# Optimization experiments

Hardware: AMD Instinct MI355X
Metric: run time of the kernel (lower is better)

Reference implementation:

```python
import jax, jax.numpy as jnp
import numpy as np

N_NODES = 50000
N_EDGES = 800000
IN_DIM = 256
HID = 64
HEADS = [4, 4, 1]
N_CLASSES = 16
SLOPE = 0.2


def mish(x):
    return x * jnp.tanh(jax.nn.softplus(x))


def gat_conv(x, src, dst, W, attn_l, attn_r, bias, res_W, n_heads, d_out, act):
    """DGL GATConv (feat_drop=attn_drop=0, residual=True, bias=True).
    x: (N, F_in); src/dst: (E,) edge endpoints; message flows src -> dst.
    """
    N = x.shape[0]
    feat = (x @ W).reshape(N, n_heads, d_out)            # (N, H, D)
    el = jnp.sum(feat * attn_l, axis=-1)                 # (N, H)
    er = jnp.sum(feat * attn_r, axis=-1)                 # (N, H)
    e = jax.nn.leaky_relu(el[src] + er[dst], SLOPE)      # (E, H)
    # segment softmax over incoming edges of each dst node
    emax = jax.ops.segment_max(e, dst, num_segments=N)   # (N, H)
    ee = jnp.exp(e - emax[dst])                          # (E, H)
    denom = jax.ops.segment_sum(ee, dst, num_segments=N) # (N, H)
    a = ee / denom[dst]                                  # (E, H)
    # weighted scatter-aggregate of source features
    rst = jax.ops.segment_sum(feat[src] * a[:, :, None], dst, num_segments=N)  # (N, H, D)
    # residual: identity if F_in == H*D else linear projection (DGL semantics)
    if res_W is None:
        res = x.reshape(N, n_heads, d_out)
    else:
        res = (x @ res_W).reshape(N, n_heads, d_out)
    rst = rst + res + bias.reshape(1, n_heads, d_out)
    if act:
        rst = mish(rst)
    return rst


def setup_inputs() -> dict:
    key = jax.random.key(0)
    ks = jax.random.split(key, 16)
    x = jax.random.normal(ks[0], (N_NODES, IN_DIM), dtype=jnp.float32)
    src = jax.random.randint(ks[1], (N_EDGES,), 0, N_NODES, dtype=jnp.int32)
    dst = jax.random.randint(ks[2], (N_EDGES,), 0, N_NODES, dtype=jnp.int32)
    s = 0.1
    # layer 0: 256 -> 4 heads x 64
    W0 = jax.random.normal(ks[3], (IN_DIM, HEADS[0] * HID), jnp.float32) * s
    al0 = jax.random.normal(ks[4], (HEADS[0], HID), jnp.float32) * s
    ar0 = jax.random.normal(ks[5], (HEADS[0], HID), jnp.float32) * s
    b0 = jnp.zeros((HEADS[0] * HID,), jnp.float32)
    # layer 1: 256 -> 4 heads x 64
    W1 = jax.random.normal(ks[6], (HEADS[0] * HID, HEADS[1] * HID), jnp.float32) * s
    al1 = jax.random.normal(ks[7], (HEADS[1], HID), jnp.float32) * s
    ar1 = jax.random.normal(ks[8], (HEADS[1], HID), jnp.float32) * s
    b1 = jnp.zeros((HEADS[1] * HID,), jnp.float32)
    # output layer: 256 -> 1 head x 16 (residual needs a linear projection)
    W2 = jax.random.normal(ks[9], (HEADS[1] * HID, HEADS[2] * N_CLASSES), jnp.float32) * s
    al2 = jax.random.normal(ks[10], (HEADS[2], N_CLASSES), jnp.float32) * s
    ar2 = jax.random.normal(ks[11], (HEADS[2], N_CLASSES), jnp.float32) * s
    b2 = jnp.zeros((HEADS[2] * N_CLASSES,), jnp.float32)
    resW2 = jax.random.normal(ks[12], (HEADS[1] * HID, HEADS[2] * N_CLASSES), jnp.float32) * s
    return {"x": x, "src": src, "dst": dst,
            "W0": W0, "al0": al0, "ar0": ar0, "b0": b0,
            "W1": W1, "al1": al1, "ar1": ar1, "b1": b1,
            "W2": W2, "al2": al2, "ar2": ar2, "b2": b2, "resW2": resW2}


def reference(x, src, dst, W0, al0, ar0, b0, W1, al1, ar1, b1, W2, al2, ar2, b2, resW2):
    N = x.shape[0]
    h = gat_conv(x, src, dst, W0, al0, ar0, b0, None, HEADS[0], HID, True).reshape(N, -1)
    h = gat_conv(h, src, dst, W1, al1, ar1, b1, None, HEADS[1], HID, True).reshape(N, -1)
    logits = gat_conv(h, src, dst, W2, al2, ar2, b2, resW2, HEADS[2], N_CLASSES, False).mean(axis=1)
    return logits
```

## Files before the change

kernel.cpp:

```cpp
#include <hip/hip_runtime.h>
#include <cmath>
#include <type_traits>

typedef __bf16 bf16;
typedef __attribute__((ext_vector_type(8))) __bf16 bf16x8;
typedef __attribute__((ext_vector_type(4))) __bf16 bf16x4;
typedef __attribute__((ext_vector_type(4))) float f32x4;

__device__ __forceinline__ unsigned f2s(float x) {
    unsigned u = __float_as_uint(x);
    return (u & 0x80000000u) ? ~u : (u | 0x80000000u);
}
__device__ __forceinline__ float s2f(unsigned s) {
    return (s & 0x80000000u) ? __uint_as_float(s & 0x7FFFFFFFu)
                             : __uint_as_float(~s);
}

__global__ void prep_weights_kernel(const float* __restrict__ W0, const float* __restrict__ W1,
                                    const float* __restrict__ W2, const float* __restrict__ rW2,
                                    bf16* __restrict__ Wt0, bf16* __restrict__ Wt1,
                                    bf16* __restrict__ Bct) {
    const int idx = blockIdx.x * blockDim.x + threadIdx.x;
    if (idx < 65536) {
        const int k = idx >> 8, m = idx & 255;
        Wt0[m * 256 + k] = (bf16)W0[idx];
        Wt1[m * 256 + k] = (bf16)W1[idx];
    }
    if (idx < 8192) {
        const int m = idx >> 8, k = idx & 255;
        const float v = (m < 16) ? W2[k * 16 + m] : rW2[k * 16 + (m - 16)];
        Bct[idx] = (bf16)v;
    }
}

template <typename AT>
__global__ __launch_bounds__(256) void gemm_mfma_bf16(const AT* __restrict__ A,
                                                      const bf16* __restrict__ Bt,
                                                      bf16* __restrict__ Fb, int N) {
    constexpr int K = 256, BM = 128, BK = 32;
    constexpr int LDA = BK + 8;
    __shared__ bf16 As[BM * LDA];
    __shared__ bf16 Bs[BM * LDA];

    const int tid = threadIdx.x;
    const int wave = tid >> 6, lane = tid & 63;
    const int quad = lane >> 4, l16 = lane & 15;
    const int rowBase = blockIdx.y * BM;
    const int colBase = blockIdx.x * BM;
    const int m_base = (wave >> 1) * 64, n_base = (wave & 1) * 64;

    f32x4 acc[4][4] = {};

    const int sr = tid >> 1;
    const int seg = (tid & 1) << 4;

    for (int k0 = 0; k0 < K; k0 += BK) {
        {
            const int gr = rowBase + sr;
            if constexpr (std::is_same<AT, float>::value) {
                float4 f0 = {0,0,0,0}, f1 = {0,0,0,0}, f2 = {0,0,0,0}, f3 = {0,0,0,0};
                if (gr < N) {
                    const float4* Ag = (const float4*)(A + (long)gr * K + k0 + seg);
                    f0 = Ag[0]; f1 = Ag[1]; f2 = Ag[2]; f3 = Ag[3];
                }
                bf16x8 p0, p1;
                p0[0] = (bf16)f0.x; p0[1] = (bf16)f0.y; p0[2] = (bf16)f0.z; p0[3] = (bf16)f0.w;
                p0[4] = (bf16)f1.x; p0[5] = (bf16)f1.y; p0[6] = (bf16)f1.z; p0[7] = (bf16)f1.w;
                p1[0] = (bf16)f2.x; p1[1] = (bf16)f2.y; p1[2] = (bf16)f2.z; p1[3] = (bf16)f2.w;
                p1[4] = (bf16)f3.x; p1[5] = (bf16)f3.y; p1[6] = (bf16)f3.z; p1[7] = (bf16)f3.w;
                *(bf16x8*)&As[sr * LDA + seg] = p0;
                *(bf16x8*)&As[sr * LDA + seg + 8] = p1;
            } else {
                bf16x8 p0 = {}, p1 = {};
                if (gr < N) {
                    const bf16x8* Ag = (const bf16x8*)(A + (long)gr * K + k0 + seg);
                    p0 = Ag[0]; p1 = Ag[1];
                }
                *(bf16x8*)&As[sr * LDA + seg] = p0;
                *(bf16x8*)&As[sr * LDA + seg + 8] = p1;
            }
        }
        {
            const bf16x8* Bg = (const bf16x8*)(Bt + (long)(colBase + sr) * K + k0 + seg);
            *(bf16x8*)&Bs[sr * LDA + seg] = Bg[0];
            *(bf16x8*)&Bs[sr * LDA + seg + 8] = Bg[1];
        }
        __syncthreads();

        bf16x8 af[4], bfr[4];
#pragma unroll
        for (int mi = 0; mi < 4; mi++)
            af[mi] = *(const bf16x8*)&As[(m_base + mi * 16 + l16) * LDA + quad * 8];
#pragma unroll
        for (int ni = 0; ni < 4; ni++)
            bfr[ni] = *(const bf16x8*)&Bs[(n_base + ni * 16 + l16) * LDA + quad * 8];
#pragma unroll
        for (int mi = 0; mi < 4; mi++)
#pragma unroll
            for (int ni = 0; ni < 4; ni++)
                acc[mi][ni] = __builtin_amdgcn_mfma_f32_16x16x32_bf16(af[mi], bfr[ni], acc[mi][ni], 0, 0, 0);
        __syncthreads();
    }

#pragma unroll
    for (int mi = 0; mi < 4; mi++) {
#pragma unroll
        for (int r = 0; r < 4; r++) {
            const int grow = rowBase + m_base + mi * 16 + quad * 4 + r;
            if (grow < N) {
#pragma unroll
                for (int ni = 0; ni < 4; ni++) {
                    Fb[(long)grow * 256 + colBase + n_base + ni * 16 + l16] = (bf16)acc[mi][ni][r];
                }
            }
        }
    }
}

__global__ __launch_bounds__(256) void gemm_mfma_n32(const bf16* __restrict__ A,
                                                     const bf16* __restrict__ Bt,
                                                     float* __restrict__ C, int N) {
    constexpr int K = 256, BM = 128, BK = 32;
    constexpr int LDA = BK + 8;
    __shared__ bf16 As[BM * LDA];
    __shared__ bf16 Bs[32 * LDA];

    const int tid = threadIdx.x;
    const int wave = tid >> 6, lane = tid & 63;
    const int quad = lane >> 4, l16 = lane & 15;
    const int rowBase = blockIdx.x * BM;
    const int m_base = (wave >> 1) * 64, n_base = (wave & 1) * 16;

    f32x4 acc[4] = {};

    const int sr = tid >> 1;
    const int seg = (tid & 1) << 4;

    for (int k0 = 0; k0 < K; k0 += BK) {
        {
            const int gr = rowBase + sr;
            bf16x8 p0 = {}, p1 = {};
            if (gr < N) {
                const bf16x8* Ag = (const bf16x8*)(A + (long)gr * K + k0 + seg);
                p0 = Ag[0]; p1 = Ag[1];
            }
            *(bf16x8*)&As[sr * LDA + seg] = p0;
            *(bf16x8*)&As[sr * LDA + seg + 8] = p1;
        }
        if (tid < 64) {
            const int br = tid >> 1;
            const bf16x8* Bg = (const bf16x8*)(Bt + br * K + k0 + seg);
            *(bf16x8*)&Bs[br * LDA + seg] = Bg[0];
            *(bf16x8*)&Bs[br * LDA + seg + 8] = Bg[1];
        }
        __syncthreads();

        const bf16x8 bfr = *(const bf16x8*)&Bs[(n_base + l16) * LDA + quad * 8];
#pragma unroll
        for (int mi = 0; mi < 4; mi++) {
            const bf16x8 af = *(const bf16x8*)&As[(m_base + mi * 16 + l16) * LDA + quad * 8];
            acc[mi] = __builtin_amdgcn_mfma_f32_16x16x32_bf16(af, bfr, acc[mi], 0, 0, 0);
        }
        __syncthreads();
    }

#pragma unroll
    for (int mi = 0; mi < 4; mi++) {
#pragma unroll
        for (int r = 0; r < 4; r++) {
            const int grow = rowBase + m_base + mi * 16 + quad * 4 + r;
            if (grow < N) C[(long)grow * 32 + n_base + l16] = acc[mi][r];
        }
    }
}

__global__ void el_er_node_kernel(const bf16* __restrict__ feat,
                                  const float* __restrict__ al, const float* __restrict__ ar,
                                  float* __restrict__ el, float* __restrict__ er, int N) {
    const int wid = (blockIdx.x * blockDim.x + threadIdx.x) >> 6;
    const int lane = threadIdx.x & 63;
    if (wid >= N) return;
    const bf16x4 f = ((const bf16x4*)feat)[(long)wid * 64 + lane];
    const float4 a = ((const float4*)al)[lane];
    const float4 b = ((const float4*)ar)[lane];
    const float f0 = (float)f[0], f1 = (float)f[1], f2 = (float)f[2], f3 = (float)f[3];
    float vl = f0 * a.x + f1 * a.y + f2 * a.z + f3 * a.w;
    float vr = f0 * b.x + f1 * b.y + f2 * b.z + f3 * b.w;
#pragma unroll
    for (int off = 1; off < 16; off <<= 1) {
        vl += __shfl_xor(vl, off);
        vr += __shfl_xor(vr, off);
    }
    if ((lane & 15) == 0) {
        const int h = lane >> 4;
        el[wid * 4 + h] = vl;
        er[wid * 4 + h] = vr;
    }
}

__global__ void el_er_strided16(const float* __restrict__ feat, int stride,
                                const float* __restrict__ al, const float* __restrict__ ar,
                                float* __restrict__ el, float* __restrict__ er, int N) {
    const int wid = (blockIdx.x * blockDim.x + threadIdx.x) >> 6;
    const int lane = threadIdx.x & 63;
    if (wid >= N) return;
    float vl = 0.f, vr = 0.f;
    if (lane < 16) {
        float f = feat[(long)wid * stride + lane];
        vl = f * al[lane];
        vr = f * ar[lane];
    }
#pragma unroll
    for (int off = 1; off < 16; off <<= 1) {
        vl += __shfl_xor(vl, off);
        vr += __shfl_xor(vr, off);
    }
    if (lane == 0) { el[wid] = vl; er[wid] = vr; }
}

__global__ void elmax4_kernel(const float4* __restrict__ el4, unsigned* __restrict__ elmax_u, int n4) {
    __shared__ float4 sm[256];
    float4 m = {-INFINITY, -INFINITY, -INFINITY, -INFINITY};
    for (int i = blockIdx.x * blockDim.x + threadIdx.x; i < n4; i += gridDim.x * blockDim.x) {
        const float4 v = el4[i];
        m.x = fmaxf(m.x, v.x); m.y = fmaxf(m.y, v.y);
        m.z = fmaxf(m.z, v.z); m.w = fmaxf(m.w, v.w);
    }
    sm[threadIdx.x] = m;
    __syncthreads();
    for (int off = 128; off > 0; off >>= 1) {
        if (threadIdx.x < off) {
            float4 o = sm[threadIdx.x + off];
            float4 c = sm[threadIdx.x];
            c.x = fmaxf(c.x, o.x); c.y = fmaxf(c.y, o.y);
            c.z = fmaxf(c.z, o.z); c.w = fmaxf(c.w, o.w);
            sm[threadIdx.x] = c;
        }
        __syncthreads();
    }
    if (threadIdx.x == 0) {
        const float4 r = sm[0];
        atomicMax(&elmax_u[0], f2s(r.x));
        atomicMax(&elmax_u[1], f2s(r.y));
        atomicMax(&elmax_u[2], f2s(r.z));
        atomicMax(&elmax_u[3], f2s(r.w));
    }
}


__global__ void count_deg_kernel(const int* __restrict__ dst, int* __restrict__ deg, int E) {
    const int e = blockIdx.x * blockDim.x + threadIdx.x;
    if (e >= E) return;
    atomicAdd(&deg[dst[e]], 1);
}

__global__ void scan_block_kernel(const int* __restrict__ deg, int* __restrict__ scanned,
                                  int* __restrict__ block_sums, int N) {
    __shared__ int smem[256];
    const int tid = threadIdx.x;
    const int base = blockIdx.x * 1024 + tid * 4;
    int v[4];
#pragma unroll
    for (int i = 0; i < 4; i++) v[i] = (base + i < N) ? deg[base + i] : 0;
    const int tsum = v[0] + v[1] + v[2] + v[3];
    smem[tid] = tsum;
    __syncthreads();
    int acc = tsum;
    for (int off = 1; off < 256; off <<= 1) {
        const int t = (tid >= off) ? smem[tid - off] : 0;
        __syncthreads();
        acc += t;
        smem[tid] = acc;
        __syncthreads();
    }
    if (tid == 255) block_sums[blockIdx.x] = acc;
    int run = acc - tsum;
#pragma unroll
    for (int i = 0; i < 4; i++) {
        if (base + i < N) scanned[base + i] = run;
        run += v[i];
    }
}

__global__ void scan_sums_kernel(int* __restrict__ block_sums, unsigned* __restrict__ elmax_u, int nb) {
    const int tid = threadIdx.x;
    if (tid < 12) elmax_u[tid] = f2s(-INFINITY);
    const int orig = (tid < nb) ? block_sums[tid] : 0;
    int v = orig;
#pragma unroll
    for (int off = 1; off < 64; off <<= 1) {
        const int t = __shfl_up(v, off);
        if (tid >= off) v += t;
    }
    if (tid < nb) block_sums[tid] = v - orig;
}

__global__ void apply_offsets_kernel(const int* __restrict__ scanned, const int* __restrict__ block_sums,
                                     int* __restrict__ row_ptr, int* __restrict__ cursor, int N, int E) {
    const int i = blockIdx.x * blockDim.x + threadIdx.x;
    if (i < N) {
        const int v = scanned[i] + block_sums[i >> 10];
        row_ptr[i] = v;
        cursor[i] = v;
    }
    if (i == 0) row_ptr[N] = E;
}

__global__ void scatter_kernel(const int* __restrict__ src, const int* __restrict__ dst,
                               int* __restrict__ cursor, int* __restrict__ csr_src, int E) {
    const int e = blockIdx.x * blockDim.x + threadIdx.x;
    if (e >= E) return;
    const int pos = atomicAdd(&cursor[dst[e]], 1);
    csr_src[pos] = src[e];
}

template <int H, int D, bool ACT, typename RT, typename OT>
__global__ void gat_aggregate_wave(const int* __restrict__ row_ptr, const int* __restrict__ csr_src,
                                   const float* __restrict__ el, const float* __restrict__ er,
                                   const unsigned* __restrict__ elmax_u,
                                   const bf16* __restrict__ feat,
                                   const RT* __restrict__ res, const float* __restrict__ bias,
                                   OT* __restrict__ out, int N) {
    constexpr int C = H * D;
    constexpr int V = C / 4;
    const int wave = threadIdx.x >> 6;
    const int lane = threadIdx.x & 63;
    int n = blockIdx.x * (blockDim.x >> 6) + wave;
    if (n >= N) return;
    n = __builtin_amdgcn_readfirstlane(n);
    const int h = lane >> 4;
    const bf16x4* feat4 = (const bf16x4*)feat;

    const float erd = er[n * H + h];
    float sh = s2f(elmax_u[h]) + erd;
    sh = (sh >= 0.f) ? sh : 0.2f * sh;

    float4 acc = {0.f, 0.f, 0.f, 0.f};
    float l = 0.f;
    int p = row_ptr[n];
    const int pend = row_ptr[n + 1];
    for (; p + 4 <= pend; p += 4) {
        const int s0 = csr_src[p + 0];
        const int s1 = csr_src[p + 1];
        const int s2 = csr_src[p + 2];
        const int s3 = csr_src[p + 3];
        float e0 = el[s0 * H + h] + erd;
        float e1 = el[s1 * H + h] + erd;
        float e2 = el[s2 * H + h] + erd;
        float e3 = el[s3 * H + h] + erd;
        e0 = (e0 >= 0.f) ? e0 : 0.2f * e0;
        e1 = (e1 >= 0.f) ? e1 : 0.2f * e1;
        e2 = (e2 >= 0.f) ? e2 : 0.2f * e2;
        e3 = (e3 >= 0.f) ? e3 : 0.2f * e3;
        const float w0 = __expf(e0 - sh);
        const float w1 = __expf(e1 - sh);
        const float w2 = __expf(e2 - sh);
        const float w3 = __expf(e3 - sh);
        const bf16x4 f0 = feat4[(long)s0 * V + lane];
        const bf16x4 f1 = feat4[(long)s1 * V + lane];
        const bf16x4 f2 = feat4[(long)s2 * V + lane];
        const bf16x4 f3 = feat4[(long)s3 * V + lane];
        l += w0 + w1 + w2 + w3;
        acc.x += w0 * (float)f0[0] + w1 * (float)f1[0] + w2 * (float)f2[0] + w3 * (float)f3[0];
        acc.y += w0 * (float)f0[1] + w1 * (float)f1[1] + w2 * (float)f2[1] + w3 * (float)f3[1];
        acc.z += w0 * (float)f0[2] + w1 * (float)f1[2] + w2 * (float)f2[2] + w3 * (float)f3[2];
        acc.w += w0 * (float)f0[3] + w1 * (float)f1[3] + w2 * (float)f2[3] + w3 * (float)f3[3];
    }
    for (; p < pend; ++p) {
        const int s = csr_src[p];
        float e = el[s * H + h] + erd;
        e = (e >= 0.f) ? e : 0.2f * e;
        const float w = __expf(e - sh);
        const bf16x4 f = feat4[(long)s * V + lane];
        l += w;
        acc.x += w * (float)f[0];
        acc.y += w * (float)f[1];
        acc.z += w * (float)f[2];
        acc.w += w * (float)f[3];
    }
    const float inv = (l > 0.f) ? 1.f / l : 0.f;
    acc.x *= inv; acc.y *= inv; acc.z *= inv; acc.w *= inv;

    float4 r;
    if constexpr (std::is_same<RT, float>::value) {
        r = ((const float4*)res)[(long)n * V + lane];
    } else {
        const bf16x4 rb = ((const bf16x4*)res)[(long)n * V + lane];
        r = make_float4((float)rb[0], (float)rb[1], (float)rb[2], (float)rb[3]);
    }
    const float4 bb = ((const float4*)bias)[lane];
    float v[4] = {acc.x + r.x + bb.x, acc.y + r.y + bb.y,
                  acc.z + r.z + bb.z, acc.w + r.w + bb.w};
    if (ACT) {
#pragma unroll
        for (int i = 0; i < 4; i++) {
            const float sp = (v[i] > 20.f) ? v[i] : log1pf(expf(v[i]));
            v[i] = v[i] * tanhf(sp);
        }
    }
    if constexpr (std::is_same<OT, float>::value) {
        float4 o = {v[0], v[1], v[2], v[3]};
        ((float4*)out)[(long)n * V + lane] = o;
    } else {
        bf16x4 o;
        o[0] = (bf16)v[0]; o[1] = (bf16)v[1]; o[2] = (bf16)v[2]; o[3] = (bf16)v[3];
        ((bf16x4*)out)[(long)n * V + lane] = o;
    }
}

template <bool ACT, int NPB>
__global__ void gat_aggregate_small(const int* __restrict__ row_ptr, const int* __restrict__ csr_src,
                                    const float* __restrict__ el, const float* __restrict__ er,
                                    const unsigned* __restrict__ elmax_u,
                                    const float* __restrict__ feat, int fstride,
                                    const float* __restrict__ res, int rstride,
                                    const float* __restrict__ bias, float* __restrict__ out, int N) {
    constexpr int C = 16;
    const int local = threadIdx.x % C;
    const int n = blockIdx.x * NPB + threadIdx.x / C;
    if (n >= N) return;
    const float mx = fmaxf(fmaxf(s2f(elmax_u[8]), s2f(elmax_u[9])),
                           fmaxf(s2f(elmax_u[10]), s2f(elmax_u[11])));
    const float erd = er[n];
    float sh = mx + erd;
    sh = (sh >= 0.f) ? sh : 0.2f * sh;

    float acc = 0.f, l = 0.f;
    int p = row_ptr[n];
    const int pend = row_ptr[n + 1];
    for (; p + 4 <= pend; p += 4) {
        const int s0 = csr_src[p + 0];
        const int s1 = csr_src[p + 1];
        const int s2 = csr_src[p + 2];
        const int s3 = csr_src[p + 3];
        float e0 = el[s0] + erd, e1 = el[s1] + erd, e2 = el[s2] + erd, e3 = el[s3] + erd;
        e0 = (e0 >= 0.f) ? e0 : 0.2f * e0;
        e1 = (e1 >= 0.f) ? e1 : 0.2f * e1;
        e2 = (e2 >= 0.f) ? e2 : 0.2f * e2;
        e3 = (e3 >= 0.f) ? e3 : 0.2f * e3;
        const float w0 = __expf(e0 - sh);
        const float w1 = __expf(e1 - sh);
        const float w2 = __expf(e2 - sh);
        const float w3 = __expf(e3 - sh);
        l += w0 + w1 + w2 + w3;
        acc += w0 * feat[(long)s0 * fstride + local] + w1 * feat[(long)s1 * fstride + local]
             + w2 * feat[(long)s2 * fstride + local] + w3 * feat[(long)s3 * fstride + local];
    }
    for (; p < pend; ++p) {
        const int s = csr_src[p];
        float e = el[s] + erd;
        e = (e >= 0.f) ? e : 0.2f * e;
        const float w = __expf(e - sh);
        l += w;
        acc += w * feat[(long)s * fstride + local];
    }
    const float inv = (l > 0.f) ? 1.f / l : 0.f;
    float v = acc * inv + res[(long)n * rstride + local] + bias[local];
    if (ACT) {
        const float sp = (v > 20.f) ? v : log1pf(expf(v));
        v = v * tanhf(sp);
    }
    out[(long)n * C + local] = v;
}


static inline int cdiv(long a, long b) { return (int)((a + b - 1) / b); }

extern "C" void kernel_launch(void* const* d_in, const int* in_sizes, int n_in,
                              void* d_out, int out_size, void* d_ws, size_t ws_size,
                              hipStream_t stream) {
    const float* x   = (const float*)d_in[0];
    const int*   src = (const int*)d_in[1];
    const int*   dst = (const int*)d_in[2];
    const float* W0  = (const float*)d_in[3];
    const float* al0 = (const float*)d_in[4];
    const float* ar0 = (const float*)d_in[5];
    const float* b0  = (const float*)d_in[6];
    const float* W1  = (const float*)d_in[7];
    const float* al1 = (const float*)d_in[8];
    const float* ar1 = (const float*)d_in[9];
    const float* b1  = (const float*)d_in[10];
    const float* W2  = (const float*)d_in[11];
    const float* al2 = (const float*)d_in[12];
    const float* ar2 = (const float*)d_in[13];
    const float* b2  = (const float*)d_in[14];
    const float* rW2 = (const float*)d_in[15];
    float* out = (float*)d_out;

    const int N = in_sizes[0] / 256;
    const int E = in_sizes[1];

    bf16* Wt0    = (bf16*)d_ws;
    bf16* Wt1    = Wt0 + 65536;
    bf16* Bct    = Wt1 + 65536;
    bf16* Fb     = Bct + 8192;
    bf16* Hb     = Fb + (long)N * 256;
    float* F2    = (float*)(Hb + (long)N * 256);
    float* el    = F2 + (long)N * 32;
    float* er    = el + (long)N * 4;
    unsigned* elmax_u = (unsigned*)(er + (long)N * 4);
    int* deg     = (int*)(elmax_u + 12);
    int* scanned = deg + N;
    int* bsums   = scanned + N;
    int* row_ptr = bsums + 64;
    int* cursor  = row_ptr + N + 1;
    int* csr_src = cursor + N;

    const int THREADS = 256;
    const int NB = cdiv(N, 1024);
    dim3 mfma_grid(2, cdiv(N, 128));

    prep_weights_kernel<<<cdiv(65536, THREADS), THREADS, 0, stream>>>(W0, W1, W2, rW2, Wt0, Wt1, Bct);
    hipMemsetAsync(deg, 0, (size_t)N * 4, stream);
    count_deg_kernel<<<cdiv(E, THREADS), THREADS, 0, stream>>>(dst, deg, E);
    scan_block_kernel<<<NB, 256, 0, stream>>>(deg, scanned, bsums, N);
    scan_sums_kernel<<<1, 64, 0, stream>>>(bsums, elmax_u, NB);
    apply_offsets_kernel<<<cdiv(N, THREADS), THREADS, 0, stream>>>(scanned, bsums, row_ptr, cursor, N, E);
    scatter_kernel<<<cdiv(E, THREADS), THREADS, 0, stream>>>(src, dst, cursor, csr_src, E);

    gemm_mfma_bf16<float><<<mfma_grid, 256, 0, stream>>>(x, Wt0, Fb, N);
    el_er_node_kernel<<<cdiv(N, 4), 256, 0, stream>>>(Fb, al0, ar0, el, er, N);
    elmax4_kernel<<<64, 256, 0, stream>>>((const float4*)el, elmax_u, N);
    gat_aggregate_wave<4, 64, true, float, bf16><<<cdiv(N, 4), 256, 0, stream>>>(
        row_ptr, csr_src, el, er, elmax_u, Fb, x, b0, Hb, N);

    gemm_mfma_bf16<bf16><<<mfma_grid, 256, 0, stream>>>(Hb, Wt1, Fb, N);
    el_er_node_kernel<<<cdiv(N, 4), 256, 0, stream>>>(Fb, al1, ar1, el, er, N);
    elmax4_kernel<<<64, 256, 0, stream>>>((const float4*)el, elmax_u + 4, N);
    gat_aggregate_wave<4, 64, true, bf16, bf16><<<cdiv(N, 4), 256, 0, stream>>>(
        row_ptr, csr_src, el, er, elmax_u + 4, Fb, Hb, b1, Hb, N);

    gemm_mfma_n32<<<cdiv(N, 128), 256, 0, stream>>>(Hb, Bct, F2, N);
    el_er_strided16<<<cdiv(N, 4), 256, 0, stream>>>(F2, 32, al2, ar2, el, er, N);
    elmax4_kernel<<<64, 256, 0, stream>>>((const float4*)el, elmax_u + 8, N / 4);
    gat_aggregate_small<false, 16><<<cdiv(N, 16), 256, 0, stream>>>(row_ptr, csr_src, el, er, elmax_u,
                                                                    F2, 32, F2 + 16, 32, b2, out, N);
}
```

Measured before the change: 477.6 us.

## Fuse el/er with max reduction, pack two nodes per wave, use exp2

Several changes land together. Attention logits are computed and max-reduced in one grid-stride kernel, which removes the separate elmax kernels. LOG2E is folded into the attention weights so the softmax can use exp2f. x is cast to bf16 once up front, and the deg memset is folded into the weight-prep kernel. The aggregation kernel now handles two destination nodes per wave with 8-wide bf16 loads, which cuts launches, global traffic and per-node wave underuse. The risks are lane divergence when the paired nodes have unequal degree, and an extra kernel plus buffer for the x cast.

```diff
diff --git a/kernel.cpp b/kernel.cpp
--- a/kernel.cpp
+++ b/kernel.cpp
@@ -7,6 +7,8 @@
 typedef __attribute__((ext_vector_type(4))) __bf16 bf16x4;
 typedef __attribute__((ext_vector_type(4))) float f32x4;
 
+#define LOG2E 1.4426950408889634f
+
 __device__ __forceinline__ unsigned f2s(float x) {
     unsigned u = __float_as_uint(x);
     return (u & 0x80000000u) ? ~u : (u | 0x80000000u);
@@ -19,7 +21,7 @@
 __global__ void prep_weights_kernel(const float* __restrict__ W0, const float* __restrict__ W1,
                                     const float* __restrict__ W2, const float* __restrict__ rW2,
                                     bf16* __restrict__ Wt0, bf16* __restrict__ Wt1,
-                                    bf16* __restrict__ Bct) {
+                                    bf16* __restrict__ Bct, int* __restrict__ deg, int N) {
     const int idx = blockIdx.x * blockDim.x + threadIdx.x;
     if (idx < 65536) {
         const int k = idx >> 8, m = idx & 255;
@@ -31,10 +33,21 @@
         const float v = (m < 16) ? W2[k * 16 + m] : rW2[k * 16 + (m - 16)];
         Bct[idx] = (bf16)v;
     }
-}
-
-template <typename AT>
-__global__ __launch_bounds__(256) void gemm_mfma_bf16(const AT* __restrict__ A,
+    if (idx < N) deg[idx] = 0;
+}
+
+__global__ void cast_x_kernel(const float* __restrict__ x, bf16* __restrict__ xb, long total8) {
+    const long t = (long)blockIdx.x * blockDim.x + threadIdx.x;
+    if (t >= total8) return;
+    const float4* xp = (const float4*)x + t * 2;
+    const float4 f0 = xp[0], f1 = xp[1];
+    bf16x8 o;
+    o[0] = (bf16)f0.x; o[1] = (bf16)f0.y; o[2] = (bf16)f0.z; o[3] = (bf16)f0.w;
+    o[4] = (bf16)f1.x; o[5] = (bf16)f1.y; o[6] = (bf16)f1.z; o[7] = (bf16)f1.w;
+    ((bf16x8*)xb)[t] = o;
+}
+
+__global__ __launch_bounds__(256) void gemm_mfma_bf16(const bf16* __restrict__ A,
                                                       const bf16* __restrict__ Bt,
                                                       bf16* __restrict__ Fb, int N) {
     constexpr int K = 256, BM = 128, BK = 32;
@@ -50,88 +63,6 @@
     const int m_base = (wave >> 1) * 64, n_base = (wave & 1) * 64;
 
     f32x4 acc[4][4] = {};
-
-    const int sr = tid >> 1;
-    const int seg = (tid & 1) << 4;
-
-    for (int k0 = 0; k0 < K; k0 += BK) {
-        {
-            const int gr = rowBase + sr;
-            if constexpr (std::is_same<AT, float>::value) {
-                float4 f0 = {0,0,0,0}, f1 = {0,0,0,0}, f2 = {0,0,0,0}, f3 = {0,0,0,0};
-                if (gr < N) {
-                    const float4* Ag = (const float4*)(A + (long)gr * K + k0 + seg);
-                    f0 = Ag[0]; f1 = Ag[1]; f2 = Ag[2]; f3 = Ag[3];
-                }
-                bf16x8 p0, p1;
-                p0[0] = (bf16)f0.x; p0[1] = (bf16)f0.y; p0[2] = (bf16)f0.z; p0[3] = (bf16)f0.w;
-                p0[4] = (bf16)f1.x; p0[5] = (bf16)f1.y; p0[6] = (bf16)f1.z; p0[7] = (bf16)f1.w;
-                p1[0] = (bf16)f2.x; p1[1] = (bf16)f2.y; p1[2] = (bf16)f2.z; p1[3] = (bf16)f2.w;
-                p1[4] = (bf16)f3.x; p1[5] = (bf16)f3.y; p1[6] = (bf16)f3.z; p1[7] = (bf16)f3.w;
-                *(bf16x8*)&As[sr * LDA + seg] = p0;
-                *(bf16x8*)&As[sr * LDA + seg + 8] = p1;
-            } else {
-                bf16x8 p0 = {}, p1 = {};
-                if (gr < N) {
-                    const bf16x8* Ag = (const bf16x8*)(A + (long)gr * K + k0 + seg);
-                    p0 = Ag[0]; p1 = Ag[1];
-                }
-                *(bf16x8*)&As[sr * LDA + seg] = p0;
-                *(bf16x8*)&As[sr * LDA + seg + 8] = p1;
-            }
-        }
-        {
-            const bf16x8* Bg = (const bf16x8*)(Bt + (long)(colBase + sr) * K + k0 + seg);
-            *(bf16x8*)&Bs[sr * LDA + seg] = Bg[0];
-            *(bf16x8*)&Bs[sr * LDA + seg + 8] = Bg[1];
-        }
-        __syncthreads();
-
-        bf16x8 af[4], bfr[4];
-#pragma unroll
-        for (int mi = 0; mi < 4; mi++)
-            af[mi] = *(const bf16x8*)&As[(m_base + mi * 16 + l16) * LDA + quad * 8];
-#pragma unroll
-        for (int ni = 0; ni < 4; ni++)
-            bfr[ni] = *(const bf16x8*)&Bs[(n_base + ni * 16 + l16) * LDA + quad * 8];
-#pragma unroll
-        for (int mi = 0; mi < 4; mi++)
-#pragma unroll
-            for (int ni = 0; ni < 4; ni++)
-                acc[mi][ni] = __builtin_amdgcn_mfma_f32_16x16x32_bf16(af[mi], bfr[ni], acc[mi][ni], 0, 0, 0);
-        __syncthreads();
-    }
-
-#pragma unroll
-    for (int mi = 0; mi < 4; mi++) {
-#pragma unroll
-        for (int r = 0; r < 4; r++) {
-            const int grow = rowBase + m_base + mi * 16 + quad * 4 + r;
-            if (grow < N) {
-#pragma unroll
-                for (int ni = 0; ni < 4; ni++) {
-                    Fb[(long)grow * 256 + colBase + n_base + ni * 16 + l16] = (bf16)acc[mi][ni][r];
-                }
-            }
-        }
-    }
-}
-
-__global__ __launch_bounds__(256) void gemm_mfma_n32(const bf16* __restrict__ A,
-                                                     const bf16* __restrict__ Bt,
-                                                     float* __restrict__ C, int N) {
-    constexpr int K = 256, BM = 128, BK = 32;
-    constexpr int LDA = BK + 8;
-    __shared__ bf16 As[BM * LDA];
-    __shared__ bf16 Bs[32 * LDA];
-
-    const int tid = threadIdx.x;
-    const int wave = tid >> 6, lane = tid & 63;
-    const int quad = lane >> 4, l16 = lane & 15;
-    const int rowBase = blockIdx.x * BM;
-    const int m_base = (wave >> 1) * 64, n_base = (wave & 1) * 16;
-
-    f32x4 acc[4] = {};
 
     const int sr = tid >> 1;
     const int seg = (tid & 1) << 4;
@@ -147,6 +78,73 @@
             *(bf16x8*)&As[sr * LDA + seg] = p0;
             *(bf16x8*)&As[sr * LDA + seg + 8] = p1;
         }
+        {
+            const bf16x8* Bg = (const bf16x8*)(Bt + (long)(colBase + sr) * K + k0 + seg);
+            *(bf16x8*)&Bs[sr * LDA + seg] = Bg[0];
+            *(bf16x8*)&Bs[sr * LDA + seg + 8] = Bg[1];
+        }
+        __syncthreads();
+
+        bf16x8 af[4], bfr[4];
+#pragma unroll
+        for (int mi = 0; mi < 4; mi++)
+            af[mi] = *(const bf16x8*)&As[(m_base + mi * 16 + l16) * LDA + quad * 8];
+#pragma unroll
+        for (int ni = 0; ni < 4; ni++)
+            bfr[ni] = *(const bf16x8*)&Bs[(n_base + ni * 16 + l16) * LDA + quad * 8];
+#pragma unroll
+        for (int mi = 0; mi < 4; mi++)
+#pragma unroll
+            for (int ni = 0; ni < 4; ni++)
+                acc[mi][ni] = __builtin_amdgcn_mfma_f32_16x16x32_bf16(af[mi], bfr[ni], acc[mi][ni], 0, 0, 0);
+        __syncthreads();
+    }
+
+#pragma unroll
+    for (int mi = 0; mi < 4; mi++) {
+#pragma unroll
+        for (int r = 0; r < 4; r++) {
+            const int grow = rowBase + m_base + mi * 16 + quad * 4 + r;
+            if (grow < N) {
+#pragma unroll
+                for (int ni = 0; ni < 4; ni++) {
+                    Fb[(long)grow * 256 + colBase + n_base + ni * 16 + l16] = (bf16)acc[mi][ni][r];
+                }
+            }
+        }
+    }
+}
+
+__global__ __launch_bounds__(256) void gemm_mfma_n32(const bf16* __restrict__ A,
+                                                     const bf16* __restrict__ Bt,
+                                                     float* __restrict__ C, int N) {
+    constexpr int K = 256, BM = 128, BK = 32;
+    constexpr int LDA = BK + 8;
+    __shared__ bf16 As[BM * LDA];
+    __shared__ bf16 Bs[32 * LDA];
+
+    const int tid = threadIdx.x;
+    const int wave = tid >> 6, lane = tid & 63;
+    const int quad = lane >> 4, l16 = lane & 15;
+    const int rowBase = blockIdx.x * BM;
+    const int m_base = (wave >> 1) * 64, n_base = (wave & 1) * 16;
+
+    f32x4 acc[4] = {};
+
+    const int sr = tid >> 1;
+    const int seg = (tid & 1) << 4;
+
+    for (int k0 = 0; k0 < K; k0 += BK) {
+        {
+            const int gr = rowBase + sr;
+            bf16x8 p0 = {}, p1 = {};
+            if (gr < N) {
+                const bf16x8* Ag = (const bf16x8*)(A + (long)gr * K + k0 + seg);
+                p0 = Ag[0]; p1 = Ag[1];
+            }
+            *(bf16x8*)&As[sr * LDA + seg] = p0;
+            *(bf16x8*)&As[sr * LDA + seg + 8] = p1;
+        }
         if (tid < 64) {
             const int br = tid >> 1;
             const bf16x8* Bg = (const bf16x8*)(Bt + br * K + k0 + seg);
@@ -174,76 +172,82 @@
     }
 }
 
-__global__ void el_er_node_kernel(const bf16* __restrict__ feat,
-                                  const float* __restrict__ al, const float* __restrict__ ar,
-                                  float* __restrict__ el, float* __restrict__ er, int N) {
-    const int wid = (blockIdx.x * blockDim.x + threadIdx.x) >> 6;
+__global__ void el_er_fused(const bf16* __restrict__ feat,
+                            const float* __restrict__ al, const float* __restrict__ ar,
+                            float* __restrict__ el, float* __restrict__ er,
+                            unsigned* __restrict__ elmax_u, int N) {
+    __shared__ float smax[16];
+    const int wave = threadIdx.x >> 6;
     const int lane = threadIdx.x & 63;
-    if (wid >= N) return;
-    const bf16x4 f = ((const bf16x4*)feat)[(long)wid * 64 + lane];
-    const float4 a = ((const float4*)al)[lane];
-    const float4 b = ((const float4*)ar)[lane];
-    const float f0 = (float)f[0], f1 = (float)f[1], f2 = (float)f[2], f3 = (float)f[3];
-    float vl = f0 * a.x + f1 * a.y + f2 * a.z + f3 * a.w;
-    float vr = f0 * b.x + f1 * b.y + f2 * b.z + f3 * b.w;
-#pragma unroll
-    for (int off = 1; off < 16; off <<= 1) {
-        vl += __shfl_xor(vl, off);
-        vr += __shfl_xor(vr, off);
-    }
-    if ((lane & 15) == 0) {
-        const int h = lane >> 4;
-        el[wid * 4 + h] = vl;
-        er[wid * 4 + h] = vr;
-    }
-}
-
-__global__ void el_er_strided16(const float* __restrict__ feat, int stride,
-                                const float* __restrict__ al, const float* __restrict__ ar,
-                                float* __restrict__ el, float* __restrict__ er, int N) {
-    const int wid = (blockIdx.x * blockDim.x + threadIdx.x) >> 6;
+    const int h = lane >> 4;
+    float4 a = ((const float4*)al)[lane];
+    float4 b = ((const float4*)ar)[lane];
+    a.x *= LOG2E; a.y *= LOG2E; a.z *= LOG2E; a.w *= LOG2E;
+    b.x *= LOG2E; b.y *= LOG2E; b.z *= LOG2E; b.w *= LOG2E;
+    const int nwaves = (gridDim.x * blockDim.x) >> 6;
+    float mloc = -INFINITY;
+    for (int wid = (blockIdx.x * blockDim.x + threadIdx.x) >> 6; wid < N; wid += nwaves) {
+        const bf16x4 f = ((const bf16x4*)feat)[(long)wid * 64 + lane];
+        const float f0 = (float)f[0], f1 = (float)f[1], f2 = (float)f[2], f3 = (float)f[3];
+        float vl = f0 * a.x + f1 * a.y + f2 * a.z + f3 * a.w;
+        float vr = f0 * b.x + f1 * b.y + f2 * b.z + f3 * b.w;
+#pragma unroll
+        for (int off = 1; off < 16; off <<= 1) {
+            vl += __shfl_xor(vl, off);
+            vr += __shfl_xor(vr, off);
+        }
+        if ((lane & 15) == 0) {
+            el[wid * 4 + h] = vl;
+            er[wid * 4 + h] = vr;
+            mloc = fmaxf(mloc, vl);
+        }
+    }
+    if ((lane & 15) == 0) smax[wave * 4 + h] = mloc;
+    __syncthreads();
+    if (threadIdx.x < 4) {
+        const float m = fmaxf(fmaxf(smax[threadIdx.x], smax[4 + threadIdx.x]),
+                              fmaxf(smax[8 + threadIdx.x], smax[12 + threadIdx.x]));
+        atomicMax(&elmax_u[threadIdx.x], f2s(m));
+    }
+}
+
+__global__ void el_er2_fused(const float* __restrict__ F2,
+                             const float* __restrict__ al2, const float* __restrict__ ar2,
+                             float* __restrict__ el, float* __restrict__ er,
+                             unsigned* __restrict__ elmax_u, int N) {
+    __shared__ float smax[4];
+    const int wave = threadIdx.x >> 6;
     const int lane = threadIdx.x & 63;
-    if (wid >= N) return;
-    float vl = 0.f, vr = 0.f;
-    if (lane < 16) {
-        float f = feat[(long)wid * stride + lane];
-        vl = f * al[lane];
-        vr = f * ar[lane];
-    }
-#pragma unroll
-    for (int off = 1; off < 16; off <<= 1) {
-        vl += __shfl_xor(vl, off);
-        vr += __shfl_xor(vr, off);
-    }
-    if (lane == 0) { el[wid] = vl; er[wid] = vr; }
-}
-
-__global__ void elmax4_kernel(const float4* __restrict__ el4, unsigned* __restrict__ elmax_u, int n4) {
-    __shared__ float4 sm[256];
-    float4 m = {-INFINITY, -INFINITY, -INFINITY, -INFINITY};
-    for (int i = blockIdx.x * blockDim.x + threadIdx.x; i < n4; i += gridDim.x * blockDim.x) {
-        const float4 v = el4[i];
-        m.x = fmaxf(m.x, v.x); m.y = fmaxf(m.y, v.y);
-        m.z = fmaxf(m.z, v.z); m.w = fmaxf(m.w, v.w);
-    }
-    sm[threadIdx.x] = m;
+    const int sub = lane >> 4;
+    const int c = lane & 15;
+    const float a = al2[c] * LOG2E;
+    const float b = ar2[c] * LOG2E;
+    const int nwaves = (gridDim.x * blockDim.x) >> 6;
+    float mloc = -INFINITY;
+    for (int q = (blockIdx.x * blockDim.x + threadIdx.x) >> 6; q * 4 < N; q += nwaves) {
+        const int n = q * 4 + sub;
+        float vl = 0.f, vr = 0.f;
+        if (n < N) {
+            const float f = F2[(long)n * 32 + c];
+            vl = f * a; vr = f * b;
+        }
+#pragma unroll
+        for (int off = 1; off < 16; off <<= 1) {
+            vl += __shfl_xor(vl, off);
+            vr += __shfl_xor(vr, off);
+        }
+        if (c == 0 && n < N) {
+            el[n] = vl; er[n] = vr;
+            mloc = fmaxf(mloc, vl);
+        }
+    }
+    mloc = fmaxf(mloc, __shfl_xor(mloc, 16));
+    mloc = fmaxf(mloc, __shfl_xor(mloc, 32));
+    if (lane == 0) smax[wave] = mloc;
     __syncthreads();
-    for (int off = 128; off > 0; off >>= 1) {
-        if (threadIdx.x < off) {
-            float4 o = sm[threadIdx.x + off];
-            float4 c = sm[threadIdx.x];
-            c.x = fmaxf(c.x, o.x); c.y = fmaxf(c.y, o.y);
-            c.z = fmaxf(c.z, o.z); c.w = fmaxf(c.w, o.w);
-            sm[threadIdx.x] = c;
-        }
-        __syncthreads();
-    }
     if (threadIdx.x == 0) {
-        const float4 r = sm[0];
-        atomicMax(&elmax_u[0], f2s(r.x));
-        atomicMax(&elmax_u[1], f2s(r.y));
-        atomicMax(&elmax_u[2], f2s(r.z));
-        atomicMax(&elmax_u[3], f2s(r.w));
+        const float m = fmaxf(fmaxf(smax[0], smax[1]), fmaxf(smax[2], smax[3]));
+        atomicMax(&elmax_u[8], f2s(m));
     }
 }
 
@@ -314,97 +318,105 @@
     csr_src[pos] = src[e];
 }
 
-template <int H, int D, bool ACT, typename RT, typename OT>
-__global__ void gat_aggregate_wave(const int* __restrict__ row_ptr, const int* __restrict__ csr_src,
-                                   const float* __restrict__ el, const float* __restrict__ er,
-                                   const unsigned* __restrict__ elmax_u,
-                                   const bf16* __restrict__ feat,
-                                   const RT* __restrict__ res, const float* __restrict__ bias,
-                                   OT* __restrict__ out, int N) {
-    constexpr int C = H * D;
-    constexpr int V = C / 4;
+template <bool ACT>
+__global__ void gat_aggregate_wave2(const int* __restrict__ row_ptr, const int* __restrict__ csr_src,
+                                    const float* __restrict__ el, const float* __restrict__ er,
+                                    const unsigned* __restrict__ elmax_u,
+                                    const bf16* __restrict__ feat,
+                                    const bf16* __restrict__ res, const float* __restrict__ bias,
+                                    bf16* __restrict__ out, int N, int E) {
     const int wave = threadIdx.x >> 6;
     const int lane = threadIdx.x & 63;
-    int n = blockIdx.x * (blockDim.x >> 6) + wave;
-    if (n >= N) return;
-    n = __builtin_amdgcn_readfirstlane(n);
-    const int h = lane >> 4;
-    const bf16x4* feat4 = (const bf16x4*)feat;
-
-    const float erd = er[n * H + h];
+    const int half = lane >> 5;
+    const int li   = lane & 31;
+    const int h    = li >> 3;
+    int nA = (blockIdx.x * (blockDim.x >> 6) + wave) * 2;
+    if (nA >= N) return;
+    nA = __builtin_amdgcn_readfirstlane(nA);
+    const int nB = nA + 1;
+    const bool haveB = (nB < N);
+    const int n = half ? (haveB ? nB : nA) : nA;
+
+    const float erd = er[n * 4 + h];
     float sh = s2f(elmax_u[h]) + erd;
-    sh = (sh >= 0.f) ? sh : 0.2f * sh;
-
-    float4 acc = {0.f, 0.f, 0.f, 0.f};
+    sh = fmaxf(sh, 0.2f * sh);
+
+    const int pA0 = row_ptr[nA];
+    const int pA1 = row_ptr[nA + 1];
+    const int pB0 = haveB ? row_ptr[nB] : 0;
+    const int pB1 = haveB ? row_ptr[nB + 1] : 0;
+    const int degA = pA1 - pA0, degB = pB1 - pB0;
+    const int steps = (degA > degB) ? degA : degB;
+    const int deg = half ? degB : degA;
+
+    const bf16x8* feat8 = (const bf16x8*)feat;
+    float acc[8] = {};
     float l = 0.f;
-    int p = row_ptr[n];
-    const int pend = row_ptr[n + 1];
-    for (; p + 4 <= pend; p += 4) {
-        const int s0 = csr_src[p + 0];
-        const int s1 = csr_src[p + 1];
-        const int s2 = csr_src[p + 2];
-        const int s3 = csr_src[p + 3];
-        float e0 = el[s0 * H + h] + erd;
-        float e1 = el[s1 * H + h] + erd;
-        float e2 = el[s2 * H + h] + erd;
-        float e3 = el[s3 * H + h] + erd;
-        e0 = (e0 >= 0.f) ? e0 : 0.2f * e0;
-        e1 = (e1 >= 0.f) ? e1 : 0.2f * e1;
-        e2 = (e2 >= 0.f) ? e2 : 0.2f * e2;
-        e3 = (e3 >= 0.f) ? e3 : 0.2f * e3;
-        const float w0 = __expf(e0 - sh);
-        const float w1 = __expf(e1 - sh);
-        const float w2 = __expf(e2 - sh);
-        const float w3 = __expf(e3 - sh);
-        const bf16x4 f0 = feat4[(long)s0 * V + lane];
-        const bf16x4 f1 = feat4[(long)s1 * V + lane];
-        const bf16x4 f2 = feat4[(long)s2 * V + lane];
-        const bf16x4 f3 = feat4[(long)s3 * V + lane];
-        l += w0 + w1 + w2 + w3;
-        acc.x += w0 * (float)f0[0] + w1 * (float)f1[0] + w2 * (float)f2[0] + w3 * (float)f3[0];
-        acc.y += w0 * (float)f0[1] + w1 * (float)f1[1] + w2 * (float)f2[1] + w3 * (float)f3[1];
-        acc.z += w0 * (float)f0[2] + w1 * (float)f1[2] + w2 * (float)f2[2] + w3 * (float)f3[2];
-        acc.w += w0 * (float)f0[3] + w1 * (float)f1[3] + w2 * (float)f2[3] + w3 * (float)f3[3];
-    }
-    for (; p < pend; ++p) {
-        const int s = csr_src[p];
-        float e = el[s * H + h] + erd;
-        e = (e >= 0.f) ? e : 0.2f * e;
-        const float w = __expf(e - sh);
-        const bf16x4 f = feat4[(long)s * V + lane];
+
+    int i = 0;
+    for (; i + 2 <= steps; i += 2) {
+        const int iA0 = min(pA0 + i, E - 1);
+        const int iB0 = min(pB0 + i, E - 1);
+        const int iA1 = min(pA0 + i + 1, E - 1);
+        const int iB1 = min(pB0 + i + 1, E - 1);
+        const int sA0 = csr_src[iA0], sB0 = csr_src[iB0];
+        const int sA1 = csr_src[iA1], sB1 = csr_src[iB1];
+        const int s0 = half ? sB0 : sA0;
+        const int s1 = half ? sB1 : sA1;
+        float e0 = el[s0 * 4 + h] + erd;
+        float e1 = el[s1 * 4 + h] + erd;
+        e0 = fmaxf(e0, 0.2f * e0);
+        e1 = fmaxf(e1, 0.2f * e1);
+        float w0 = exp2f(e0 - sh);
+        float w1 = exp2f(e1 - sh);
+        w0 = (i < deg) ? w0 : 0.f;
+        w1 = (i + 1 < deg) ? w1 : 0.f;
+        const bf16x8 f0 = feat8[(long)s0 * 32 + li];
+        const bf16x8 f1 = feat8[(long)s1 * 32 + li];
+        l += w0 + w1;
+#pragma unroll
+        for (int j = 0; j < 8; j++) acc[j] += w0 * (float)f0[j] + w1 * (float)f1[j];
+    }
+    for (; i < steps; ++i) {
+        const int iA = min(pA0 + i, E - 1);
+        const int iB = min(pB0 + i, E - 1);
+        const int sA = csr_src[iA], sB = csr_src[iB];
+        const int s = half ? sB : sA;
+        float e = el[s * 4 + h] + erd;
+        e = fmaxf(e, 0.2f * e);
+        float w = exp2f(e - sh);
+        w = (i < deg) ? w : 0.f;
+        const bf16x8 f = feat8[(long)s * 32 + li];
         l += w;
-        acc.x += w * (float)f[0];
-        acc.y += w * (float)f[1];
-        acc.z += w * (float)f[2];
-        acc.w += w * (float)f[3];
+#pragma unroll
+        for (int j = 0; j < 8; j++) acc[j] += w * (float)f[j];
     }
     const float inv = (l > 0.f) ? 1.f / l : 0.f;
-    acc.x *= inv; acc.y *= inv; acc.z *= inv; acc.w *= inv;
-
-    float4 r;
-    if constexpr (std::is_same<RT, float>::value) {
-        r = ((const float4*)res)[(long)n * V + lane];
-    } else {
-        const bf16x4 rb = ((const bf16x4*)res)[(long)n * V + lane];
-        r = make_float4((float)rb[0], (float)rb[1], (float)rb[2], (float)rb[3]);
-    }
-    const float4 bb = ((const float4*)bias)[lane];
-    float v[4] = {acc.x + r.x + bb.x, acc.y + r.y + bb.y,
-                  acc.z + r.z + bb.z, acc.w + r.w + bb.w};
+
+    const bf16x8 rb = ((const bf16x8*)res)[(long)n * 32 + li];
+    const float4 bb0 = ((const float4*)bias)[li * 2];
+    const float4 bb1 = ((const float4*)bias)[li * 2 + 1];
+    float v[8];
+    v[0] = acc[0] * inv + (float)rb[0] + bb0.x;
+    v[1] = acc[1] * inv + (float)rb[1] + bb0.y;
+    v[2] = acc[2] * inv + (float)rb[2] + bb0.z;
+    v[3] = acc[3] * inv + (float)rb[3] + bb0.w;
+    v[4] = acc[4] * inv + (float)rb[4] + bb1.x;
+    v[5] = acc[5] * inv + (float)rb[5] + bb1.y;
+    v[6] = acc[6] * inv + (float)rb[6] + bb1.z;
+    v[7] = acc[7] * inv + (float)rb[7] + bb1.w;
     if (ACT) {
 #pragma unroll
-        for (int i = 0; i < 4; i++) {
-            const float sp = (v[i] > 20.f) ? v[i] : log1pf(expf(v[i]));
-            v[i] = v[i] * tanhf(sp);
-        }
-    }
-    if constexpr (std::is_same<OT, float>::value) {
-        float4 o = {v[0], v[1], v[2], v[3]};
-        ((float4*)out)[(long)n * V + lane] = o;
-    } else {
-        bf16x4 o;
-        o[0] = (bf16)v[0]; o[1] = (bf16)v[1]; o[2] = (bf16)v[2]; o[3] = (bf16)v[3];
-        ((bf16x4*)out)[(long)n * V + lane] = o;
+        for (int j = 0; j < 8; j++) {
+            const float sp = (v[j] > 20.f) ? v[j] : log1pf(expf(v[j]));
+            v[j] = v[j] * tanhf(sp);
+        }
+    }
+    if (half == 0 || haveB) {
+        bf16x8 o;
+#pragma unroll
+        for (int j = 0; j < 8; j++) o[j] = (bf16)v[j];
+        ((bf16x8*)out)[(long)n * 32 + li] = o;
     }
 }
 
@@ -419,11 +431,10 @@
     const int local = threadIdx.x % C;
     const int n = blockIdx.x * NPB + threadIdx.x / C;
     if (n >= N) return;
-    const float mx = fmaxf(fmaxf(s2f(elmax_u[8]), s2f(elmax_u[9])),
-                           fmaxf(s2f(elmax_u[10]), s2f(elmax_u[11])));
+    const float mx = s2f(elmax_u[8]);
     const float erd = er[n];
     float sh = mx + erd;
-    sh = (sh >= 0.f) ? sh : 0.2f * sh;
+    sh = fmaxf(sh, 0.2f * sh);
 
     float acc = 0.f, l = 0.f;
     int p = row_ptr[n];
@@ -434,14 +445,14 @@
         const int s2 = csr_src[p + 2];
         const int s3 = csr_src[p + 3];
         float e0 = el[s0] + erd, e1 = el[s1] + erd, e2 = el[s2] + erd, e3 = el[s3] + erd;
-        e0 = (e0 >= 0.f) ? e0 : 0.2f * e0;
-        e1 = (e1 >= 0.f) ? e1 : 0.2f * e1;
-        e2 = (e2 >= 0.f) ? e2 : 0.2f * e2;
-        e3 = (e3 >= 0.f) ? e3 : 0.2f * e3;
-        const float w0 = __expf(e0 - sh);
-        const float w1 = __expf(e1 - sh);
-        const float w2 = __expf(e2 - sh);
-        const float w3 = __expf(e3 - sh);
+        e0 = fmaxf(e0, 0.2f * e0);
+        e1 = fmaxf(e1, 0.2f * e1);
+        e2 = fmaxf(e2, 0.2f * e2);
+        e3 = fmaxf(e3, 0.2f * e3);
+        const float w0 = exp2f(e0 - sh);
+        const float w1 = exp2f(e1 - sh);
+        const float w2 = exp2f(e2 - sh);
+        const float w3 = exp2f(e3 - sh);
         l += w0 + w1 + w2 + w3;
         acc += w0 * feat[(long)s0 * fstride + local] + w1 * feat[(long)s1 * fstride + local]
              + w2 * feat[(long)s2 * fstride + local] + w3 * feat[(long)s3 * fstride + local];
@@ -449,8 +460,8 @@
     for (; p < pend; ++p) {
         const int s = csr_src[p];
         float e = el[s] + erd;
-        e = (e >= 0.f) ? e : 0.2f * e;
-        const float w = __expf(e - sh);
+        e = fmaxf(e, 0.2f * e);
+        const float w = exp2f(e - sh);
         l += w;
         acc += w * feat[(long)s * fstride + local];
     }
@@ -493,7 +504,8 @@
     bf16* Wt0    = (bf16*)d_ws;
     bf16* Wt1    = Wt0 + 65536;
     bf16* Bct    = Wt1 + 65536;
-    bf16* Fb     = Bct + 8192;
+    bf16* xb     = Bct + 8192;
+    bf16* Fb     = xb + (long)N * 256;
     bf16* Hb     = Fb + (long)N * 256;
     float* F2    = (float*)(Hb + (long)N * 256);
     float* el    = F2 + (long)N * 32;
@@ -510,29 +522,26 @@
     const int NB = cdiv(N, 1024);
     dim3 mfma_grid(2, cdiv(N, 128));
 
-    prep_weights_kernel<<<cdiv(65536, THREADS), THREADS, 0, stream>>>(W0, W1, W2, rW2, Wt0, Wt1, Bct);
-    hipMemsetAsync(deg, 0, (size_t)N * 4, stream);
+    prep_weights_kernel<<<cdiv(65536, THREADS), THREADS, 0, stream>>>(W0, W1, W2, rW2, Wt0, Wt1, Bct, deg, N);
+    cast_x_kernel<<<cdiv((long)N * 32, THREADS), THREADS, 0, stream>>>(x, xb, (long)N * 32);
     count_deg_kernel<<<cdiv(E, THREADS), THREADS, 0, stream>>>(dst, deg, E);
     scan_block_kernel<<<NB, 256, 0, stream>>>(deg, scanned, bsums, N);
     scan_sums_kernel<<<1, 64, 0, stream>>>(bsums, elmax_u, NB);
     apply_offsets_kernel<<<cdiv(N, THREADS), THREADS, 0, stream>>>(scanned, bsums, row_ptr, cursor, N, E);
     scatter_kernel<<<cdiv(E, THREADS), THREADS, 0, stream>>>(src, dst, cursor, csr_src, E);
 
-    gemm_mfma_bf16<float><<<mfma_grid, 256, 0, stream>>>(x, Wt0, Fb, N);
-    el_er_node_kernel<<<cdiv(N, 4), 256, 0, stream>>>(Fb, al0, ar0, el, er, N);
-    elmax4_kernel<<<64, 256, 0, stream>>>((const float4*)el, elmax_u, N);
-    gat_aggregate_wave<4, 64, true, float, bf16><<<cdiv(N, 4), 256, 0, stream>>>(
-        row_ptr, csr_src, el, er, elmax_u, Fb, x, b0, Hb, N);
-
-    gemm_mfma_bf16<bf16><<<mfma_grid, 256, 0, stream>>>(Hb, Wt1, Fb, N);
-    el_er_node_kernel<<<cdiv(N, 4), 256, 0, stream>>>(Fb, al1, ar1, el, er, N);
-    elmax4_kernel<<<64, 256, 0, stream>>>((const float4*)el, elmax_u + 4, N);
-    gat_aggregate_wave<4, 64, true, bf16, bf16><<<cdiv(N, 4), 256, 0, stream>>>(
-        row_ptr, csr_src, el, er, elmax_u + 4, Fb, Hb, b1, Hb, N);
+    gemm_mfma_bf16<<<mfma_grid, 256, 0, stream>>>(xb, Wt0, Fb, N);
+    el_er_fused<<<256, 256, 0, stream>>>(Fb, al0, ar0, el, er, elmax_u, N);
+    gat_aggregate_wave2<true><<<cdiv(N, 8), 256, 0, stream>>>(
+        row_ptr, csr_src, el, er, elmax_u, Fb, xb, b0, Hb, N, E);
+
+    gemm_mfma_bf16<<<mfma_grid, 256, 0, stream>>>(Hb, Wt1, Fb, N);
+    el_er_fused<<<256, 256, 0, stream>>>(Fb, al1, ar1, el, er, elmax_u + 4, N);
+    gat_aggregate_wave2<true><<<cdiv(N, 8), 256, 0, stream>>>(
+        row_ptr, csr_src, el, er, elmax_u + 4, Fb, Hb, b1, Hb, N, E);
 
     gemm_mfma_n32<<<cdiv(N, 128), 256, 0, stream>>>(Hb, Bct, F2, N);
-    el_er_strided16<<<cdiv(N, 4), 256, 0, stream>>>(F2, 32, al2, ar2, el, er, N);
-    elmax4_kernel<<<64, 256, 0, stream>>>((const float4*)el, elmax_u + 8, N / 4);
+    el_er2_fused<<<128, 256, 0, stream>>>(F2, al2, ar2, el, er, elmax_u, N);
     gat_aggregate_small<false, 16><<<cdiv(N, 16), 256, 0, stream>>>(row_ptr, csr_src, el, er, elmax_u,
                                                                     F2, 32, F2 + 16, 32, b2, out, N);
 }
```

Measured after the change: 525.1 us. 9.9% more time.
